# Kernel tuning notes

Hardware: AMD Instinct MI355X
Metric: run time of the kernel (lower is better)

Reference implementation:

```python
import jax, jax.numpy as jnp
import numpy as np

NEG_INF = -9e15


def setup_inputs() -> dict:
    key = jax.random.key(0)
    k1, k2, k3, k4, k5, k6 = jax.random.split(key, 6)
    B, N, F_IN, F_OUT = 16, 2048, 256, 128
    inputs = jax.random.normal(k1, (B, N, F_IN), dtype=jnp.float32)
    adj_matrix = jax.random.randint(k2, (B, N, N), 0, 2, dtype=jnp.int32)
    W = jax.random.normal(k3, (F_OUT, F_IN), dtype=jnp.float32) * (1.0 / np.sqrt(F_IN))
    b_W = jax.random.normal(k4, (F_OUT,), dtype=jnp.float32) * 0.02
    a = jax.random.normal(k5, (1, 2 * F_OUT), dtype=jnp.float32) * (1.0 / np.sqrt(2 * F_OUT))
    b_a = jax.random.normal(k6, (1,), dtype=jnp.float32) * 0.02
    return {"inputs": inputs, "adj_matrix": adj_matrix, "W": W, "b_W": b_W, "a": a, "b_a": b_a}


def reference(inputs, adj_matrix, W, b_W, a, b_a):
    # wh: [B, N, H]
    wh = jnp.einsum('bnf,hf->bnh', inputs, W) + b_W
    H = wh.shape[-1]
    # linear_self_W([wh_i, wh_j]) = a1.wh_i + a2.wh_j + b  (rank-1 linear over concat)
    a1 = a[0, :H]
    a2 = a[0, H:]
    src = jnp.einsum('bnh,h->bn', wh, a1)  # [B, N] contribution of row node i
    dst = jnp.einsum('bnh,h->bn', wh, a2)  # [B, N] contribution of col node j
    e = jax.nn.leaky_relu(src[:, :, None] + dst[:, None, :] + b_a[0], negative_slope=0.01)
    e = jnp.where(adj_matrix > 0, e, NEG_INF)
    att = jax.nn.softmax(e, axis=-1)  # dropout in eval mode = identity
    return jax.nn.elu(jnp.einsum('bij,bjh->bih', att, wh))
```

## Files before the change

### kernel.cpp

```cpp
#include <hip/hip_runtime.h>


#define BDIM 16
#define NDIM 2048
#define FIN 256
#define HDIM 128
#define LOG2E 1.4426950408889634f

typedef short short8 __attribute__((ext_vector_type(8)));
typedef float floatx4 __attribute__((ext_vector_type(4)));
typedef int intx4 __attribute__((ext_vector_type(4)));

__device__ __forceinline__ unsigned short f2bf(float x) {
    unsigned int u = __float_as_uint(x);
    unsigned int r = (u + 0x7fffu + ((u >> 16) & 1u)) >> 16;
    return (unsigned short)r;
}
__device__ __forceinline__ float bf2f(unsigned short s) {
    return __uint_as_float(((unsigned int)s) << 16);
}
__device__ __forceinline__ intx4 ldnt(const int* p) {
    return __builtin_nontemporal_load(reinterpret_cast<const intx4*>(p));
}

__global__ __launch_bounds__(256) void k_wh(const float* __restrict__ X,
                                            const float* __restrict__ W,
                                            const float* __restrict__ bW,
                                            const float* __restrict__ a,
                                            const float* __restrict__ ba_p,
                                            float* __restrict__ src,
                                            float* __restrict__ dst,
                                            unsigned short* __restrict__ whF) {
    __shared__ short lds[27648];
    short (*ah)[72] = (short(*)[72])lds;
    short (*al)[72] = (short(*)[72])(lds + 4608);
    short (*bh)[72] = (short(*)[72])(lds + 9216);
    short (*bl)[72] = (short(*)[72])(lds + 18432);
    short (*tb)[72] = (short(*)[72])lds;

    const int tid = threadIdx.x;
    const long row0 = (long)blockIdx.x * 64;
    const int w = tid >> 6, lane = tid & 63;
    const int lm = lane & 15, q = lane >> 4;
    const float ba0 = ba_p[0];

    float a1v[8], a2v[8], bwv[8];
    #pragma unroll
    for (int nt = 0; nt < 8; nt++) {
        a1v[nt] = a[nt * 16 + lm];
        a2v[nt] = a[HDIM + nt * 16 + lm];
        bwv[nt] = bW[nt * 16 + lm];
    }

    floatx4 acc[8];
    #pragma unroll
    for (int nt = 0; nt < 8; nt++) acc[nt] = (floatx4){0.f, 0.f, 0.f, 0.f};

    for (int k0 = 0; k0 < FIN; k0 += 64) {
        #pragma unroll
        for (int u = 0; u < 4; u++) {
            int idx = tid + u * 256;
            int r = idx >> 4, fc = (idx & 15) * 4;
            float4 v = *reinterpret_cast<const float4*>(X + (row0 + r) * FIN + k0 + fc);
            union { unsigned short s[4]; uint2 u2; } ph, pl;
            ph.s[0] = f2bf(v.x); pl.s[0] = f2bf(v.x - bf2f(ph.s[0]));
            ph.s[1] = f2bf(v.y); pl.s[1] = f2bf(v.y - bf2f(ph.s[1]));
            ph.s[2] = f2bf(v.z); pl.s[2] = f2bf(v.z - bf2f(ph.s[2]));
            ph.s[3] = f2bf(v.w); pl.s[3] = f2bf(v.w - bf2f(ph.s[3]));
            *reinterpret_cast<uint2*>(&ah[r][fc]) = ph.u2;
            *reinterpret_cast<uint2*>(&al[r][fc]) = pl.u2;
        }
        #pragma unroll
        for (int u = 0; u < 8; u++) {
            int idx = tid + u * 256;
            int hh = idx >> 4, fc = (idx & 15) * 4;
            float4 v = *reinterpret_cast<const float4*>(W + hh * FIN + k0 + fc);
            union { unsigned short s[4]; uint2 u2; } ph, pl;
            ph.s[0] = f2bf(v.x); pl.s[0] = f2bf(v.x - bf2f(ph.s[0]));
            ph.s[1] = f2bf(v.y); pl.s[1] = f2bf(v.y - bf2f(ph.s[1]));
            ph.s[2] = f2bf(v.z); pl.s[2] = f2bf(v.z - bf2f(ph.s[2]));
            ph.s[3] = f2bf(v.w); pl.s[3] = f2bf(v.w - bf2f(ph.s[3]));
            *reinterpret_cast<uint2*>(&bh[hh][fc]) = ph.u2;
            *reinterpret_cast<uint2*>(&bl[hh][fc]) = pl.u2;
        }
        __syncthreads();
        #pragma unroll
        for (int ks = 0; ks < 64; ks += 32) {
            short8 afh = *reinterpret_cast<const short8*>(&ah[w * 16 + lm][ks + q * 8]);
            short8 afl = *reinterpret_cast<const short8*>(&al[w * 16 + lm][ks + q * 8]);
            #pragma unroll
            for (int nt = 0; nt < 8; nt++) {
                short8 bfh = *reinterpret_cast<const short8*>(&bh[nt * 16 + lm][ks + q * 8]);
                short8 bfl = *reinterpret_cast<const short8*>(&bl[nt * 16 + lm][ks + q * 8]);
                acc[nt] = __builtin_amdgcn_mfma_f32_16x16x32_bf16(afh, bfh, acc[nt], 0, 0, 0);
                acc[nt] = __builtin_amdgcn_mfma_f32_16x16x32_bf16(afh, bfl, acc[nt], 0, 0, 0);
                acc[nt] = __builtin_amdgcn_mfma_f32_16x16x32_bf16(afl, bfh, acc[nt], 0, 0, 0);
            }
        }
        __syncthreads();
    }

    float s1[4] = {0.f, 0.f, 0.f, 0.f}, s2[4] = {0.f, 0.f, 0.f, 0.f};
    #pragma unroll
    for (int nt = 0; nt < 8; nt++) {
        #pragma unroll
        for (int r = 0; r < 4; r++) {
            float v = acc[nt][r] + bwv[nt];
            s1[r] += v * a1v[nt];
            s2[r] += v * a2v[nt];
            tb[nt * 16 + lm][w * 16 + q * 4 + r] = f2bf(v);
        }
    }
    #pragma unroll
    for (int r = 0; r < 4; r++) {
        #pragma unroll
        for (int o = 1; o < 16; o <<= 1) {
            s1[r] += __shfl_xor(s1[r], o);
            s2[r] += __shfl_xor(s2[r], o);
        }
    }
    if (lm == 0) {
        #pragma unroll
        for (int r = 0; r < 4; r++) {
            long row = row0 + w * 16 + q * 4 + r;
            src[row] = (s1[r] + ba0) * LOG2E;
            dst[row] = s2[r] * LOG2E;
        }
    }
    __syncthreads();
    const int b = (int)(row0 >> 11);
    const int jc0 = (int)((row0 & 2047) >> 5);
    const int f = tid >> 4;
    const int sub = tid & 15;
    const int jcrel = f >> 3, ht = f & 7;
    const size_t fbase = (((size_t)b * 64 + jc0 + jcrel) * 8 + ht) * 512;
    #pragma unroll
    for (int i = 0; i < 4; i++) {
        int l = sub * 4 + i;
        uint4 v = *reinterpret_cast<const uint4*>(&tb[ht * 16 + (l & 15)][jcrel * 32 + (l >> 4) * 8]);
        *reinterpret_cast<uint4*>(whF + fbase + l * 8) = v;
    }
}


#define CHUNK(T, P, PW)                                                        \
    do {                                                                       \
        if ((T) < NDIM / 32 - 3) {          \
            const int* ap = adjp + ((T) + 3) * 32;                             \
            m[((P) + 3) & 3][0] = ldnt(ap);                                    \
            m[((P) + 3) & 3][1] = ldnt(ap + 4);                                \
        }                                                                      \
        if ((T) < NDIM / 32 - 1) {         \
            const float* dp = dstp + ((T) + 1) * 32;                           \
            d[(PW) ^ 1][0] = *reinterpret_cast<const floatx4*>(dp);            \
            d[(PW) ^ 1][1] = *reinterpret_cast<const floatx4*>(dp + 4);        \
            const unsigned short* wp = whFb + (size_t)((T) + 1) * 8 * 512;     \
            _Pragma("unroll")                                                  \
            for (int hj = 0; hj < 8; hj++)                                     \
                bfr[(PW) ^ 1][hj] =                                            \
                    *reinterpret_cast<const short8*>(wp + hj * 512);           \
        }                                                                      \
        short8 af;                                                             \
        _Pragma("unroll")                                                      \
        for (int j = 0; j < 8; j++) {                                          \
            float x = si + d[(PW)][j >> 2][j & 3];                             \
            x = fmaxf(x, 0.01f * x);               \
            float wgt = m[(P)][j >> 2][j & 3] > 0                              \
                            ? __builtin_amdgcn_exp2f(x)                        \
                            : 0.f;                                             \
            lpart += wgt;                                                      \
            af[j] = (short)f2bf(wgt);                                          \
        }                                                                      \
        _Pragma("unroll")                                                      \
        for (int hj = 0; hj < 8; hj++)                                         \
            acc[hj] = __builtin_amdgcn_mfma_f32_16x16x32_bf16(af, bfr[(PW)][hj], \
                                                              acc[hj], 0, 0, 0); \
    } while (0)

__global__ __launch_bounds__(256) void k_attn(const int* __restrict__ adj,
                                              const unsigned short* __restrict__ whF,
                                              const float* __restrict__ src,
                                              const float* __restrict__ dst,
                                              float* __restrict__ out) {
    __shared__ float lred[64];
    __shared__ float linv_s[64];

    const int tid = threadIdx.x;
    const int bid = ((int)blockIdx.x & 7) * 64 + ((int)blockIdx.x >> 3);
    const int b = bid >> 5;
    const int i0 = (bid & 31) * 64;
    const int wave = tid >> 6, lane = tid & 63;
    const int lm = lane & 15, q = lane >> 4;
    const int irow = i0 + wave * 16 + lm;

    const float si = src[b * NDIM + irow];
    const int* adjp = adj + ((size_t)(b * NDIM + irow)) * NDIM + q * 8;
    const float* dstp = dst + b * NDIM + q * 8;
    const unsigned short* whFb = whF + (size_t)b * 64 * 8 * 512 + lane * 8;

    floatx4 acc[8];
    #pragma unroll
    for (int hj = 0; hj < 8; hj++) acc[hj] = (floatx4){0.f, 0.f, 0.f, 0.f};
    float lpart = 0.f;

    intx4 m[4][2];
    floatx4 d[2][2];
    short8 bfr[2][8];
    m[0][0] = ldnt(adjp);       m[0][1] = ldnt(adjp + 4);
    m[1][0] = ldnt(adjp + 32);  m[1][1] = ldnt(adjp + 36);
    m[2][0] = ldnt(adjp + 64);  m[2][1] = ldnt(adjp + 68);
    d[0][0] = *reinterpret_cast<const floatx4*>(dstp);
    d[0][1] = *reinterpret_cast<const floatx4*>(dstp + 4);
    #pragma unroll
    for (int hj = 0; hj < 8; hj++) bfr[0][hj] = *reinterpret_cast<const short8*>(whFb + hj * 512);

    for (int t = 0; t < NDIM / 32; t += 4) {
        CHUNK(t + 0, 0, 0);
        CHUNK(t + 1, 1, 1);
        CHUNK(t + 2, 2, 0);
        CHUNK(t + 3, 3, 1);
    }

    lpart += __shfl_xor(lpart, 16);
    lpart += __shfl_xor(lpart, 32);
    if (q == 0) lred[wave * 16 + lm] = lpart;
    __syncthreads();
    if (tid < 64) {
        float l = lred[tid];
        linv_s[tid] = l > 0.f ? 1.f / l : 0.f;
    }
    __syncthreads();

    #pragma unroll
    for (int r = 0; r < 4; r++) {
        int il = wave * 16 + q * 4 + r;
        float li = linv_s[il];
        size_t obase = ((size_t)(b * NDIM + i0 + il)) * HDIM + lm;
        #pragma unroll
        for (int hj = 0; hj < 8; hj++) {
            float x = acc[hj][r] * li;
            x = x > 0.f ? x : (__expf(x) - 1.f);
            out[obase + hj * 16] = x;
        }
    }
}

extern "C" void kernel_launch(void* const* d_in, const int* in_sizes, int n_in,
                              void* d_out, int out_size, void* d_ws, size_t ws_size,
                              hipStream_t stream) {
    const float* X  = (const float*)d_in[0];
    const int* adj  = (const int*)d_in[1];
    const float* W  = (const float*)d_in[2];
    const float* bW = (const float*)d_in[3];
    const float* a  = (const float*)d_in[4];
    const float* ba = (const float*)d_in[5];
    float* out = (float*)d_out;

    float* srcv = (float*)d_ws;
    float* dstv = srcv + BDIM * NDIM;
    unsigned short* whF = (unsigned short*)(dstv + BDIM * NDIM);

    k_wh<<<BDIM * NDIM / 64, 256, 0, stream>>>(X, W, bW, a, ba, srcv, dstv, whF);
    k_attn<<<BDIM * (NDIM / 64), 256, 0, stream>>>(adj, whF, srcv, dstv, out);
}
```

Before: 436.4 us.

## Pack adjacency into bitmask in projection kernel, consume bits in attention

The projection kernel now also reads the int32 adjacency matrix and packs it into a 1-bit-per-edge mask with wave ballots, written to workspace. The attention kernel reads 32-bit mask words instead of streaming int32 adjacency entries, which simplifies its prefetch pipeline and frees registers. The full adjacency read still happens once, now in the first kernel. The mask write and reread are small, but the packing loop has a single lane doing the stores, which may serialize the first kernel and add latency.

```diff
diff --git a/kernel.cpp b/kernel.cpp
--- a/kernel.cpp
+++ b/kernel.cpp
@@ -9,7 +9,6 @@
 
 typedef short short8 __attribute__((ext_vector_type(8)));
 typedef float floatx4 __attribute__((ext_vector_type(4)));
-typedef int intx4 __attribute__((ext_vector_type(4)));
 
 __device__ __forceinline__ unsigned short f2bf(float x) {
     unsigned int u = __float_as_uint(x);
@@ -19,18 +18,17 @@
 __device__ __forceinline__ float bf2f(unsigned short s) {
     return __uint_as_float(((unsigned int)s) << 16);
 }
-__device__ __forceinline__ intx4 ldnt(const int* p) {
-    return __builtin_nontemporal_load(reinterpret_cast<const intx4*>(p));
-}
 
 __global__ __launch_bounds__(256) void k_wh(const float* __restrict__ X,
+                                            const int* __restrict__ adj,
                                             const float* __restrict__ W,
                                             const float* __restrict__ bW,
                                             const float* __restrict__ a,
                                             const float* __restrict__ ba_p,
                                             float* __restrict__ src,
                                             float* __restrict__ dst,
-                                            unsigned short* __restrict__ whF) {
+                                            unsigned short* __restrict__ whF,
+                                            unsigned* __restrict__ maskG) {
     __shared__ short lds[27648];
     short (*ah)[72] = (short(*)[72])lds;
     short (*al)[72] = (short(*)[72])(lds + 4608);
@@ -140,34 +138,49 @@
         uint4 v = *reinterpret_cast<const uint4*>(&tb[ht * 16 + (l & 15)][jcrel * 32 + (l >> 4) * 8]);
         *reinterpret_cast<uint4*>(whF + fbase + l * 8) = v;
     }
-}
-
-
-#define CHUNK(T, P, PW)                                                        \
+
+    {
+        #pragma unroll 1
+        for (int ri = 0; ri < 16; ri++) {
+            const size_t gr = (size_t)row0 + w * 16 + ri;
+            const int* ar = adj + gr * NDIM + lane;
+            unsigned* mo = maskG + gr * 64;
+            #pragma unroll 8
+            for (int ci = 0; ci < 32; ci++) {
+                int v = __builtin_nontemporal_load(ar + ci * 64);
+                unsigned long long bal = __ballot(v != 0);
+                if (lane == 0) {
+                    uint2 pk;
+                    pk.x = (unsigned)bal;
+                    pk.y = (unsigned)(bal >> 32);
+                    *reinterpret_cast<uint2*>(mo + ci * 2) = pk;
+                }
+            }
+        }
+    }
+}
+
+#define CH(T, PW)                                                              \
     do {                                                                       \
-        if ((T) < NDIM / 32 - 3) {          \
-            const int* ap = adjp + ((T) + 3) * 32;                             \
-            m[((P) + 3) & 3][0] = ldnt(ap);                                    \
-            m[((P) + 3) & 3][1] = ldnt(ap + 4);                                \
-        }                                                                      \
-        if ((T) < NDIM / 32 - 1) {         \
+        if ((T) < NDIM / 32 - 1) {        \
             const float* dp = dstp + ((T) + 1) * 32;                           \
             d[(PW) ^ 1][0] = *reinterpret_cast<const floatx4*>(dp);            \
             d[(PW) ^ 1][1] = *reinterpret_cast<const floatx4*>(dp + 4);        \
+            md[(PW) ^ 1] = mrow[(T) + 1];                                      \
             const unsigned short* wp = whFb + (size_t)((T) + 1) * 8 * 512;     \
             _Pragma("unroll")                                                  \
             for (int hj = 0; hj < 8; hj++)                                     \
                 bfr[(PW) ^ 1][hj] =                                            \
                     *reinterpret_cast<const short8*>(wp + hj * 512);           \
         }                                                                      \
+        const unsigned ms = md[(PW)] >> q8;       \
         short8 af;                                                             \
         _Pragma("unroll")                                                      \
         for (int j = 0; j < 8; j++) {                                          \
             float x = si + d[(PW)][j >> 2][j & 3];                             \
             x = fmaxf(x, 0.01f * x);               \
-            float wgt = m[(P)][j >> 2][j & 3] > 0                              \
-                            ? __builtin_amdgcn_exp2f(x)                        \
-                            : 0.f;                                             \
+            float e2 = __builtin_amdgcn_exp2f(x);                              \
+            float wgt = (ms & (1u << j)) ? e2 : 0.f;                           \
             lpart += wgt;                                                      \
             af[j] = (short)f2bf(wgt);                                          \
         }                                                                      \
@@ -177,7 +190,7 @@
                                                               acc[hj], 0, 0, 0); \
     } while (0)
 
-__global__ __launch_bounds__(256) void k_attn(const int* __restrict__ adj,
+__global__ __launch_bounds__(256) void k_attn(const unsigned* __restrict__ maskG,
                                               const unsigned short* __restrict__ whF,
                                               const float* __restrict__ src,
                                               const float* __restrict__ dst,
@@ -191,11 +204,12 @@
     const int i0 = (bid & 31) * 64;
     const int wave = tid >> 6, lane = tid & 63;
     const int lm = lane & 15, q = lane >> 4;
+    const int q8 = q * 8;
     const int irow = i0 + wave * 16 + lm;
 
     const float si = src[b * NDIM + irow];
-    const int* adjp = adj + ((size_t)(b * NDIM + irow)) * NDIM + q * 8;
-    const float* dstp = dst + b * NDIM + q * 8;
+    const unsigned* mrow = maskG + (size_t)(b * NDIM + irow) * 64;
+    const float* dstp = dst + b * NDIM + q8;
     const unsigned short* whFb = whF + (size_t)b * 64 * 8 * 512 + lane * 8;
 
     floatx4 acc[8];
@@ -203,22 +217,18 @@
     for (int hj = 0; hj < 8; hj++) acc[hj] = (floatx4){0.f, 0.f, 0.f, 0.f};
     float lpart = 0.f;
 
-    intx4 m[4][2];
+    unsigned md[2];
     floatx4 d[2][2];
     short8 bfr[2][8];
-    m[0][0] = ldnt(adjp);       m[0][1] = ldnt(adjp + 4);
-    m[1][0] = ldnt(adjp + 32);  m[1][1] = ldnt(adjp + 36);
-    m[2][0] = ldnt(adjp + 64);  m[2][1] = ldnt(adjp + 68);
+    md[0] = mrow[0];
     d[0][0] = *reinterpret_cast<const floatx4*>(dstp);
     d[0][1] = *reinterpret_cast<const floatx4*>(dstp + 4);
     #pragma unroll
     for (int hj = 0; hj < 8; hj++) bfr[0][hj] = *reinterpret_cast<const short8*>(whFb + hj * 512);
 
-    for (int t = 0; t < NDIM / 32; t += 4) {
-        CHUNK(t + 0, 0, 0);
-        CHUNK(t + 1, 1, 1);
-        CHUNK(t + 2, 2, 0);
-        CHUNK(t + 3, 3, 1);
+    for (int t = 0; t < NDIM / 32; t += 2) {
+        CH(t + 0, 0);
+        CH(t + 1, 1);
     }
 
     lpart += __shfl_xor(lpart, 16);
@@ -259,7 +269,8 @@
     float* srcv = (float*)d_ws;
     float* dstv = srcv + BDIM * NDIM;
     unsigned short* whF = (unsigned short*)(dstv + BDIM * NDIM);
-
-    k_wh<<<BDIM * NDIM / 64, 256, 0, stream>>>(X, W, bW, a, ba, srcv, dstv, whF);
-    k_attn<<<BDIM * (NDIM / 64), 256, 0, stream>>>(adj, whF, srcv, dstv, out);
-}
+    unsigned* maskG = (unsigned*)(whF + (size_t)BDIM * NDIM * HDIM);
+
+    k_wh<<<BDIM * NDIM / 64, 256, 0, stream>>>(X, adj, W, bW, a, ba, srcv, dstv, whF, maskG);
+    k_attn<<<BDIM * (NDIM / 64), 256, 0, stream>>>(maskG, whF, srcv, dstv, out);
+}
```

After: 605.3 us. +38.7%, slower.

## Warp-specialize attention kernel with producer waves staging wh tiles and adjacency bitmasks

Applied to the files above, without the earlier changes.

Doubles the block to 512 threads, split into four consumer waves that do the exp and MFMA work and four producer waves. The producers load the bf16 wh tiles into double-buffered shared memory and read the int32 adjacency rows coalesced. They pack those rows into bitmasks with ballots and store them in shared memory. The aim is to spread the adjacency stream over dedicated waves, cut per-lane mask registers, and share the wh tiles through LDS instead of each wave reloading them. In exchange it adds a __syncthreads per 32-column chunk and more LDS use, which may reduce occupancy.

```diff
diff --git a/kernel.cpp b/kernel.cpp
--- a/kernel.cpp
+++ b/kernel.cpp
@@ -143,45 +143,112 @@
 }
 
 
-#define CHUNK(T, P, PW)                                                        \
-    do {                                                                       \
-        if ((T) < NDIM / 32 - 3) {          \
-            const int* ap = adjp + ((T) + 3) * 32;                             \
-            m[((P) + 3) & 3][0] = ldnt(ap);                                    \
-            m[((P) + 3) & 3][1] = ldnt(ap + 4);                                \
-        }                                                                      \
-        if ((T) < NDIM / 32 - 1) {         \
-            const float* dp = dstp + ((T) + 1) * 32;                           \
-            d[(PW) ^ 1][0] = *reinterpret_cast<const floatx4*>(dp);            \
-            d[(PW) ^ 1][1] = *reinterpret_cast<const floatx4*>(dp + 4);        \
-            const unsigned short* wp = whFb + (size_t)((T) + 1) * 8 * 512;     \
-            _Pragma("unroll")                                                  \
-            for (int hj = 0; hj < 8; hj++)                                     \
-                bfr[(PW) ^ 1][hj] =                                            \
-                    *reinterpret_cast<const short8*>(wp + hj * 512);           \
-        }                                                                      \
+#define MD_PRE(PW1, BK, HI)                                                    \
+    do {                                                                       \
+        md[PW1][0] = maskB[BK][0 + (HI)][wrow];                                \
+        md[PW1][1] = maskB[BK][2 + (HI)][wrow];                                \
+        md[PW1][2] = maskB[BK][4 + (HI)][wrow];                                \
+        md[PW1][3] = maskB[BK][6 + (HI)][wrow];                                \
+    } while (0)
+
+#define ADJ_ISSUE(GNEXT, H)                                                    \
+    do {                                                                       \
+        _Pragma("unroll")                                                      \
+        for (int r = 0; r < 8; r++) {                                          \
+            const int* ap = adj +                                              \
+                (size_t)(rowbase + cw * 16 + (H) * 8 + r) * NDIM +             \
+                (GNEXT) * 256 + lane * 4;                                      \
+            av[r] = ldnt(ap);                                                  \
+        }                                                                      \
+    } while (0)
+
+#define ADJ_BALLOT(GNEXT, H)                                                   \
+    do {                                                                       \
+        _Pragma("unroll")                                                      \
+        for (int r = 0; r < 8; r++) {                                          \
+            unsigned long long b0 = __ballot(av[r][0] != 0);                   \
+            unsigned long long b1 = __ballot(av[r][1] != 0);                   \
+            unsigned long long b2 = __ballot(av[r][2] != 0);                   \
+            unsigned long long b3 = __ballot(av[r][3] != 0);                   \
+            if (lane < 8) {                                                    \
+                unsigned long long bb = (lane < 2) ? b0                        \
+                                        : (lane < 4) ? b1                      \
+                                        : (lane < 6) ? b2 : b3;                \
+                unsigned wv = (lane & 1) ? (unsigned)(bb >> 32) : (unsigned)bb;\
+                maskB[(GNEXT) & 1][lane][cw * 16 + (H) * 8 + r] = wv;          \
+            }                                                                  \
+        }                                                                      \
+    } while (0)
+
+#define CHC(C)                                                                 \
+    do {                                                                       \
+        constexpr int PW = (C) & 1;                                            \
+        const int T = g8 + (C);                                                \
+        if (!(g8 == 56 && (C) == 7)) {                       \
+            const float* dp = dstp + (T + 1) * 32;                             \
+            d[PW ^ 1][0] = *reinterpret_cast<const floatx4*>(dp);              \
+            d[PW ^ 1][1] = *reinterpret_cast<const floatx4*>(dp + 4);          \
+            if ((C) < 7) {                                                     \
+                MD_PRE(PW ^ 1, (g8 >> 3) & 1, (((C) + 1) & 4) ? 1 : 0);        \
+            } else {                                                           \
+                MD_PRE(PW ^ 1, ((g8 >> 3) + 1) & 1, 0);                        \
+            }                                                                  \
+        }                                                                      \
+        const int base = 8 * ((C) & 3) + 2 * q;                                \
         short8 af;                                                             \
         _Pragma("unroll")                                                      \
         for (int j = 0; j < 8; j++) {                                          \
-            float x = si + d[(PW)][j >> 2][j & 3];                             \
+            float x = si + d[PW][j >> 2][j & 3];                               \
             x = fmaxf(x, 0.01f * x);               \
-            float wgt = m[(P)][j >> 2][j & 3] > 0                              \
-                            ? __builtin_amdgcn_exp2f(x)                        \
-                            : 0.f;                                             \
+            float e2 = __builtin_amdgcn_exp2f(x);                              \
+            unsigned bit = (md[PW][j & 3] >> (base + (j >> 2))) & 1u;          \
+            float wgt = bit ? e2 : 0.f;                                        \
             lpart += wgt;                                                      \
             af[j] = (short)f2bf(wgt);                                          \
         }                                                                      \
         _Pragma("unroll")                                                      \
-        for (int hj = 0; hj < 8; hj++)                                         \
-            acc[hj] = __builtin_amdgcn_mfma_f32_16x16x32_bf16(af, bfr[(PW)][hj], \
+        for (int hj = 0; hj < 8; hj++) {                                       \
+            short8 fb = *reinterpret_cast<const short8*>(                      \
+                &whS[PW][hj * 512 + lane * 8]);                                \
+            acc[hj] = __builtin_amdgcn_mfma_f32_16x16x32_bf16(af, fb,          \
                                                               acc[hj], 0, 0, 0); \
-    } while (0)
-
-__global__ __launch_bounds__(256) void k_attn(const int* __restrict__ adj,
+        }                                                                      \
+    } while (0)
+
+#define CHP(C)                                                                 \
+    do {                                                                       \
+        constexpr int PW = (C) & 1;                                            \
+        const int T = g8 + (C);                                                \
+        if (T + 2 < 64) {                   \
+            const unsigned short* gp = gsrc + (size_t)(T + 2) * 4096;          \
+            sr[PW][0] = *reinterpret_cast<const short8*>(gp);                  \
+            sr[PW][1] = *reinterpret_cast<const short8*>(gp + 512);            \
+        }                                                                      \
+        if ((C) == 0 && g8 < 56) ADJ_ISSUE((g8 >> 3) + 1, 0);                  \
+        if ((C) == 3 && g8 < 56) {                                             \
+            ADJ_BALLOT((g8 >> 3) + 1, 0);                                      \
+            ADJ_ISSUE((g8 >> 3) + 1, 1);                                       \
+        }                                                                      \
+        if ((C) == 6 && g8 < 56) ADJ_BALLOT((g8 >> 3) + 1, 1);                 \
+        if (T + 1 < 64) {                 \
+            *reinterpret_cast<short8*>(&whS[PW ^ 1][pofs]) = sr[PW ^ 1][0];    \
+            *reinterpret_cast<short8*>(&whS[PW ^ 1][pofs + 512]) = sr[PW ^ 1][1]; \
+        }                                                                      \
+    } while (0)
+
+#define ITER(C)                                                                \
+    do {                                                                       \
+        if (wave < 4) { CHC(C); } else { CHP(C); }                             \
+        __syncthreads();                                                       \
+    } while (0)
+
+__global__ __launch_bounds__(512) void k_attn(const int* __restrict__ adj,
                                               const unsigned short* __restrict__ whF,
                                               const float* __restrict__ src,
                                               const float* __restrict__ dst,
                                               float* __restrict__ out) {
+    __shared__ short whS[2][4096];
+    __shared__ unsigned maskB[2][8][64];
     __shared__ float lred[64];
     __shared__ float linv_s[64];
 
@@ -190,40 +257,53 @@
     const int b = bid >> 5;
     const int i0 = (bid & 31) * 64;
     const int wave = tid >> 6, lane = tid & 63;
+    const int cw = wave & 3;
     const int lm = lane & 15, q = lane >> 4;
-    const int irow = i0 + wave * 16 + lm;
-
-    const float si = src[b * NDIM + irow];
-    const int* adjp = adj + ((size_t)(b * NDIM + irow)) * NDIM + q * 8;
+    const int wrow = cw * 16 + lm;
+    const int rowbase = b * NDIM + i0;
+
+    const float si = src[rowbase + wrow];
     const float* dstp = dst + b * NDIM + q * 8;
-    const unsigned short* whFb = whF + (size_t)b * 64 * 8 * 512 + lane * 8;
+    const unsigned short* gsrc =
+        whF + (size_t)b * 64 * 8 * 512 + cw * 1024 + lane * 8;
+    const int pofs = cw * 1024 + lane * 8;
 
     floatx4 acc[8];
     #pragma unroll
     for (int hj = 0; hj < 8; hj++) acc[hj] = (floatx4){0.f, 0.f, 0.f, 0.f};
     float lpart = 0.f;
 
-    intx4 m[4][2];
+    unsigned md[2][4];
     floatx4 d[2][2];
-    short8 bfr[2][8];
-    m[0][0] = ldnt(adjp);       m[0][1] = ldnt(adjp + 4);
-    m[1][0] = ldnt(adjp + 32);  m[1][1] = ldnt(adjp + 36);
-    m[2][0] = ldnt(adjp + 64);  m[2][1] = ldnt(adjp + 68);
-    d[0][0] = *reinterpret_cast<const floatx4*>(dstp);
-    d[0][1] = *reinterpret_cast<const floatx4*>(dstp + 4);
-    #pragma unroll
-    for (int hj = 0; hj < 8; hj++) bfr[0][hj] = *reinterpret_cast<const short8*>(whFb + hj * 512);
-
-    for (int t = 0; t < NDIM / 32; t += 4) {
-        CHUNK(t + 0, 0, 0);
-        CHUNK(t + 1, 1, 1);
-        CHUNK(t + 2, 2, 0);
-        CHUNK(t + 3, 3, 1);
+    short8 sr[2][2];
+    intx4 av[8];
+
+    if (wave >= 4) {
+        short8 p0 = *reinterpret_cast<const short8*>(gsrc);
+        short8 p1 = *reinterpret_cast<const short8*>(gsrc + 512);
+        *reinterpret_cast<short8*>(&whS[0][pofs]) = p0;
+        *reinterpret_cast<short8*>(&whS[0][pofs + 512]) = p1;
+        sr[1][0] = *reinterpret_cast<const short8*>(gsrc + 4096);
+        sr[1][1] = *reinterpret_cast<const short8*>(gsrc + 4096 + 512);
+        ADJ_ISSUE(0, 0);
+        ADJ_BALLOT(0, 0);
+        ADJ_ISSUE(0, 1);
+        ADJ_BALLOT(0, 1);
+    } else {
+        d[0][0] = *reinterpret_cast<const floatx4*>(dstp);
+        d[0][1] = *reinterpret_cast<const floatx4*>(dstp + 4);
+    }
+    __syncthreads();
+    if (wave < 4) MD_PRE(0, 0, 0);
+
+    for (int g8 = 0; g8 < 64; g8 += 8) {
+        ITER(0); ITER(1); ITER(2); ITER(3);
+        ITER(4); ITER(5); ITER(6); ITER(7);
     }
 
     lpart += __shfl_xor(lpart, 16);
     lpart += __shfl_xor(lpart, 32);
-    if (q == 0) lred[wave * 16 + lm] = lpart;
+    if (wave < 4 && q == 0) lred[cw * 16 + lm] = lpart;
     __syncthreads();
     if (tid < 64) {
         float l = lred[tid];
@@ -231,16 +311,18 @@
     }
     __syncthreads();
 
-    #pragma unroll
-    for (int r = 0; r < 4; r++) {
-        int il = wave * 16 + q * 4 + r;
-        float li = linv_s[il];
-        size_t obase = ((size_t)(b * NDIM + i0 + il)) * HDIM + lm;
-        #pragma unroll
-        for (int hj = 0; hj < 8; hj++) {
-            float x = acc[hj][r] * li;
-            x = x > 0.f ? x : (__expf(x) - 1.f);
-            out[obase + hj * 16] = x;
+    if (wave < 4) {
+        #pragma unroll
+        for (int r = 0; r < 4; r++) {
+            int il = cw * 16 + q * 4 + r;
+            float li = linv_s[il];
+            size_t obase = ((size_t)(rowbase + il)) * HDIM + lm;
+            #pragma unroll
+            for (int hj = 0; hj < 8; hj++) {
+                float x = acc[hj][r] * li;
+                x = x > 0.f ? x : (__expf(x) - 1.f);
+                out[obase + hj * 16] = x;
+            }
         }
     }
 }
@@ -261,5 +343,5 @@
     unsigned short* whF = (unsigned short*)(dstv + BDIM * NDIM);
 
     k_wh<<<BDIM * NDIM / 64, 256, 0, stream>>>(X, W, bW, a, ba, srcv, dstv, whF);
-    k_attn<<<BDIM * (NDIM / 64), 256, 0, stream>>>(adj, whF, srcv, dstv, out);
-}
+    k_attn<<<BDIM * (NDIM / 64), 512, 0, stream>>>(adj, whF, srcv, dstv, out);
+}
```

Result: faster. 427.8 us (-2.0%).
